# Performance work log

Hardware: AMD Instinct MI355X
Metric: run time of the kernel (lower is better)

The kernel has to match this reference:

```python
import jax, jax.numpy as jnp
import numpy as np

# Qwen3.5 GatedDeltaNet dims
B, T, HID = 2, 2048, 2048
HK, HV, DK, DV, KW = 16, 32, 128, 128, 4   # k-heads, v-heads, head dims, conv kernel
R = HV // HK                                # GQA repeat factor = 2
KEY_DIM = HK * DK                           # 2048
VAL_DIM = HV * DV                           # 4096
CONV_DIM = 2 * KEY_DIM + VAL_DIM            # 8192
EPS = 1e-6


def setup_inputs() -> dict:
    key = jax.random.key(0)
    ks = jax.random.split(key, 10)
    w = lambda k, shape, s=0.02: (jax.random.normal(k, shape) * s).astype(jnp.float32)
    A = jax.random.uniform(ks[8], (HV,), minval=1e-3, maxval=16.0)
    return {
        "hidden_states": jax.random.normal(ks[0], (B, T, HID), jnp.float32),
        "W_qkv": w(ks[1], (HID, CONV_DIM)),
        "W_z": w(ks[2], (HID, VAL_DIM)),
        "W_b": w(ks[3], (HID, HV)),
        "W_a": w(ks[4], (HID, HV)),
        "conv_w": w(ks[5], (CONV_DIM, KW), 0.5),   # depthwise causal conv taps
        "dt_bias": jnp.ones((HV,), jnp.float32),
        "A_log": jnp.log(A).astype(jnp.float32),
        "norm_weight": jnp.ones((DV,), jnp.float32),
        "W_out": w(ks[9], (VAL_DIM, HID)),
    }


def _forward(hidden_states, W_qkv, W_z, W_b, W_a, conv_w, dt_bias, A_log, norm_weight, W_out):
    x = hidden_states
    # --- projections ---
    qkv = x @ W_qkv                                    # [B,T,CONV_DIM]
    z = x @ W_z                                        # [B,T,VAL_DIM]
    beta = jax.nn.sigmoid(x @ W_b)                     # [B,T,HV]
    alpha = x @ W_a                                    # [B,T,HV]
    g = -jnp.exp(A_log) * jax.nn.softplus(alpha + dt_bias)  # [B,T,HV] (log-decay <= 0)

    # --- fix_query_key_value_ordering: per-k-head interleaved layout ---
    qkv = qkv.reshape(B, T, HK, 2 * DK + R * DV)
    q, k, v = jnp.split(qkv, [DK, 2 * DK], axis=3)
    mixed = jnp.concatenate([q.reshape(B, T, -1), k.reshape(B, T, -1), v.reshape(B, T, -1)], axis=-1)

    # --- causal depthwise short conv (kernel 4) + SiLU ---
    xp = jnp.pad(mixed, ((0, 0), (KW - 1, 0), (0, 0)))
    conv = sum(conv_w[:, i] * xp[:, i:i + T, :] for i in range(KW))
    conv = jax.nn.silu(conv)

    q, k, v = jnp.split(conv, [KEY_DIM, 2 * KEY_DIM], axis=-1)
    q = q.reshape(B, T, HK, DK)
    k = k.reshape(B, T, HK, DK)
    v = v.reshape(B, T, HV, DV)
    gate = z.reshape(B, T, HV, DV)

    # GQA: repeat q,k heads to match v heads
    q = jnp.repeat(q, R, axis=2)                       # [B,T,HV,DK]
    k = jnp.repeat(k, R, axis=2)

    # l2-norm q,k (use_qk_l2norm_in_kernel=True) and default scale 1/sqrt(DK)
    q = q / jnp.sqrt(jnp.sum(q * q, axis=-1, keepdims=True) + 1e-6)
    k = k / jnp.sqrt(jnp.sum(k * k, axis=-1, keepdims=True) + 1e-6)
    q = q * (DK ** -0.5)

    # --- gated delta rule recurrence (scan over time) ---
    # state S: [B,HV,DK,DV];  S_t = a_t*S_{t-1} + k_t (beta_t*(v_t - (a_t*S_{t-1})^T k_t))^T
    def step(S, inp):
        qt, kt, vt, gt, bt = inp                       # [B,HV,DK],[B,HV,DK],[B,HV,DV],[B,HV],[B,HV]
        S = S * jnp.exp(gt)[:, :, None, None]
        kv = jnp.einsum('bhk,bhkv->bhv', kt, S)
        delta = bt[..., None] * (vt - kv)              # [B,HV,DV]
        S = S + kt[..., None] * delta[:, :, None, :]
        o = jnp.einsum('bhk,bhkv->bhv', qt, S)
        return S, o

    tfirst = lambda a: jnp.moveaxis(a, 1, 0)           # [T,B,...]
    S0 = jnp.zeros((B, HV, DK, DV), q.dtype)
    _, o = jax.lax.scan(step, S0, (tfirst(q), tfirst(k), tfirst(v), tfirst(g), tfirst(beta)))
    o = jnp.moveaxis(o, 0, 1)                          # [B,T,HV,DV]

    # --- gated RMSNorm: rmsnorm(o) * silu(gate) * weight ---
    var = jnp.mean(o * o, axis=-1, keepdims=True)
    o = o * jax.lax.rsqrt(var + EPS)
    o = o * jax.nn.silu(gate)
    o = o * norm_weight

    return o.reshape(B, T, VAL_DIM) @ W_out            # [B,T,HID]


def reference(hidden_states, W_qkv, W_z, W_b, W_a, conv_w, dt_bias, A_log, norm_weight, W_out):
    return _forward(hidden_states, W_qkv, W_z, W_b, W_a, conv_w, dt_bias, A_log, norm_weight, W_out)
```

## Files before the change

### kernel.cpp

```cpp
#include <hip/hip_runtime.h>


#define T_LEN 2048
#define MROWS 4096

typedef __bf16 bf16x8 __attribute__((ext_vector_type(8)));
typedef float f32x4 __attribute__((ext_vector_type(4)));

#define MFMA(a, b, c) __builtin_amdgcn_mfma_f32_16x16x32_bf16((a), (b), (c), 0, 0, 0)

__device__ __forceinline__ unsigned short f2bf(float f) {
  unsigned int u = __float_as_uint(f);
  unsigned int r = (u + 0x7fffu + ((u >> 16) & 1u)) >> 16;
  return (unsigned short)r;
}
__device__ __forceinline__ float bf2f(unsigned short u) {
  return __uint_as_float(((unsigned int)u) << 16);
}
__device__ __forceinline__ void gload_lds16(const void* g, void* l) {
  __builtin_amdgcn_global_load_lds(
      (const __attribute__((address_space(1))) unsigned int*)g,
      (__attribute__((address_space(3))) unsigned int*)l, 16, 0, 0);
}

__global__ __launch_bounds__(256) void f32_to_bf16_vec(const float* __restrict__ src,
                                                       unsigned short* __restrict__ dst,
                                                       int n4) {
  int i = blockIdx.x * 256 + threadIdx.x;
  if (i >= n4) return;
  float4 v = ((const float4*)src)[i];
  ushort4 o;
  o.x = f2bf(v.x); o.y = f2bf(v.y); o.z = f2bf(v.z); o.w = f2bf(v.w);
  ((ushort4*)dst)[i] = o;
}

__global__ __launch_bounds__(256) void transpose_f2b(const float* __restrict__ src,
                                                     unsigned short* __restrict__ dst,
                                                     int R, int C) {
  __shared__ float tile[32][33];
  int tx = threadIdx.x & 31, ty = threadIdx.x >> 5;
  int c0 = blockIdx.x * 32, r0 = blockIdx.y * 32;
  #pragma unroll
  for (int i = ty; i < 32; i += 8)
    tile[i][tx] = src[(size_t)(r0 + i) * C + c0 + tx];
  __syncthreads();
  #pragma unroll
  for (int i = ty; i < 32; i += 8)
    dst[(size_t)(c0 + i) * R + r0 + tx] = f2bf(tile[tx][i]);
}

template <int OUTBF, int BN>
__global__ __launch_bounds__(512, 2) void gemm256(const unsigned short* __restrict__ A, int lda,
                                                  const unsigned short* __restrict__ Bt, int ldb,
                                                  void* __restrict__ Cv, int ldc,
                                                  int M, int N, int K) {
  constexpr int BUFSZ = 16384 + BN * 64;
  constexpr int BISS = BN / 64;
  constexpr int IS = 4 + BISS;
  constexpr int WMv = (BN == 256) ? 2 : 4;
  constexpr int MSUB = 256 / (WMv * 16);
  constexpr int MSPAN = 256 / WMv;

  __shared__ unsigned short lds[2 * BUFSZ];

  const int mtiles = M >> 8;
  const int nwg = gridDim.x;
  const int orig = blockIdx.x;
  const int q = nwg >> 3, r = nwg & 7;
  const int xcd = orig & 7, idx = orig >> 3;
  const int swz = (xcd < r ? xcd * (q + 1) : r * (q + 1) + (xcd - r) * q) + idx;
  const int m0 = (swz % mtiles) * 256;
  const int n0 = (swz / mtiles) * BN;

  const int tid = threadIdx.x, lane = tid & 63, wv = tid >> 6;
  const int wm = (BN == 256) ? (wv >> 2) : (wv >> 1);
  const int wn = (BN == 256) ? (wv & 3) : (wv & 1);
  const int l15 = lane & 15, l4 = lane >> 4;

  f32x4 acc[MSUB][4];
  #pragma unroll
  for (int i = 0; i < MSUB; i++)
    #pragma unroll
    for (int j = 0; j < 4; j++) acc[i][j] = f32x4{0.f, 0.f, 0.f, 0.f};

  const int NT = K >> 6;

  auto STAGE = [&](int kt) {
    unsigned short* base = lds + (kt & 1) * BUFSZ;
    const int k0 = kt << 6;
    #pragma unroll
    for (int is = 0; is < 4; is++) {
      int ow = is * 8192 + wv * 1024;
      int o = ow + lane * 16;
      int row = o >> 7, colB = o & 127;
      int scol = colB ^ ((row & 7) << 4);
      gload_lds16(A + (size_t)(m0 + row) * lda + k0 + (scol >> 1), base + (ow >> 1));
    }
    #pragma unroll
    for (int is = 0; is < BISS; is++) {
      int ow = is * 8192 + wv * 1024;
      int o = ow + lane * 16;
      int row = o >> 7, colB = o & 127;
      int scol = colB ^ ((row & 7) << 4);
      gload_lds16(Bt + (size_t)(n0 + row) * ldb + k0 + (scol >> 1), base + 16384 + (ow >> 1));
    }
  };

  STAGE(0);
  if (NT > 1) STAGE(1);
  if constexpr (IS == 8) asm volatile("s_waitcnt vmcnt(8)" ::: "memory");
  else                   asm volatile("s_waitcnt vmcnt(6)" ::: "memory");
  __builtin_amdgcn_sched_barrier(0);
  __builtin_amdgcn_s_barrier();
  __builtin_amdgcn_sched_barrier(0);

  for (int t = 0; t < NT; t++) {
    const unsigned short* Abuf = lds + (t & 1) * BUFSZ;
    const unsigned short* Bbuf = Abuf + 16384;
    bf16x8 bF[4][2];
    #pragma unroll
    for (int n = 0; n < 4; n++) {
      int rb = wn * 64 + n * 16 + l15;
      int sw = (rb & 7) << 4;
      #pragma unroll
      for (int ks = 0; ks < 2; ks++) {
        int colB = (ks * 32 + l4 * 8) * 2;
        bF[n][ks] = *(const bf16x8*)(Bbuf + rb * 64 + ((colB ^ sw) >> 1));
      }
    }
    __builtin_amdgcn_s_setprio(1);
    #pragma unroll
    for (int m = 0; m < MSUB; m++) {
      int ra = wm * MSPAN + m * 16 + l15;
      int sw = (ra & 7) << 4;
      int c0b = l4 * 16;
      bf16x8 a0 = *(const bf16x8*)(Abuf + ra * 64 + ((c0b ^ sw) >> 1));
      bf16x8 a1 = *(const bf16x8*)(Abuf + ra * 64 + (((64 + c0b) ^ sw) >> 1));
      #pragma unroll
      for (int n = 0; n < 4; n++) {
        acc[m][n] = MFMA(a0, bF[n][0], acc[m][n]);
        acc[m][n] = MFMA(a1, bF[n][1], acc[m][n]);
      }
    }
    __builtin_amdgcn_s_setprio(0);
    __builtin_amdgcn_sched_barrier(0);
    __builtin_amdgcn_s_barrier();
    __builtin_amdgcn_sched_barrier(0);
    if (t + 2 < NT) STAGE(t + 2);
    if (t + 1 < NT) {
      if (t + 2 < NT) {
        if constexpr (IS == 8) asm volatile("s_waitcnt vmcnt(8)" ::: "memory");
        else                   asm volatile("s_waitcnt vmcnt(6)" ::: "memory");
      } else {
        asm volatile("s_waitcnt vmcnt(0)" ::: "memory");
      }
      __builtin_amdgcn_sched_barrier(0);
      __builtin_amdgcn_s_barrier();
      __builtin_amdgcn_sched_barrier(0);
    }
  }

  #pragma unroll
  for (int m = 0; m < MSUB; m++) {
    int grow = m0 + wm * MSPAN + m * 16 + l4 * 4;
    #pragma unroll
    for (int n = 0; n < 4; n++) {
      int gcol = n0 + wn * 64 + n * 16 + l15;
      if (OUTBF) {
        unsigned short* cp = (unsigned short*)Cv + (size_t)grow * ldc + gcol;
        #pragma unroll
        for (int rr = 0; rr < 4; rr++) cp[(size_t)rr * ldc] = f2bf(acc[m][n][rr]);
      } else {
        float* cp = (float*)Cv + (size_t)grow * ldc + gcol;
        #pragma unroll
        for (int rr = 0; rr < 4; rr++) cp[(size_t)rr * ldc] = acc[m][n][rr];
      }
    }
  }
}

template <int OUTBF>
__global__ __launch_bounds__(256) void gemm_bf16(const unsigned short* __restrict__ A, int lda,
                                                 const unsigned short* __restrict__ Bt, int ldb,
                                                 void* __restrict__ Cv, int ldc,
                                                 int M, int N, int K) {
  __shared__ unsigned short As[128 * 64];
  __shared__ unsigned short Bs[128 * 64];
  const int tid = threadIdx.x, lane = tid & 63, wv = tid >> 6;
  const int wr = wv >> 1, wc = wv & 1;
  const int m0 = blockIdx.y * 128, n0 = blockIdx.x * 128;
  const int lrow8 = lane >> 3;
  const int lk8 = (lane & 7) * 8;

  f32x4 acc[4][4];
  #pragma unroll
  for (int i = 0; i < 4; i++)
    #pragma unroll
    for (int j = 0; j < 4; j++) acc[i][j] = f32x4{0.f, 0.f, 0.f, 0.f};

  for (int k0 = 0; k0 < K; k0 += 64) {
    #pragma unroll
    for (int j = 0; j < 4; ++j) {
      int chunk = j * 4 + wv;
      int r = chunk * 8 + lrow8;
      gload_lds16(A + (size_t)(m0 + r) * lda + k0 + lk8, (void*)(As + chunk * 512));
      gload_lds16(Bt + (size_t)(n0 + r) * ldb + k0 + lk8, (void*)(Bs + chunk * 512));
    }
    __syncthreads();
    #pragma unroll
    for (int half = 0; half < 2; ++half) {
      int ko = half * 32 + (lane >> 4) * 8;
      bf16x8 af[4], bfr[4];
      #pragma unroll
      for (int i = 0; i < 4; i++) {
        int ra = wr * 64 + i * 16 + (lane & 15);
        af[i] = *(const bf16x8*)(As + ra * 64 + ko);
        int rb = wc * 64 + i * 16 + (lane & 15);
        bfr[i] = *(const bf16x8*)(Bs + rb * 64 + ko);
      }
      #pragma unroll
      for (int i = 0; i < 4; i++)
        #pragma unroll
        for (int j = 0; j < 4; j++)
          acc[i][j] = MFMA(af[i], bfr[j], acc[i][j]);
    }
    __syncthreads();
  }
  int cr4 = (lane >> 4) * 4;
  int cc = lane & 15;
  #pragma unroll
  for (int i = 0; i < 4; i++) {
    int row = m0 + wr * 64 + i * 16 + cr4;
    #pragma unroll
    for (int j = 0; j < 4; j++) {
      int col = n0 + wc * 64 + j * 16 + cc;
      if (OUTBF) {
        unsigned short* cp = (unsigned short*)Cv + (size_t)row * ldc + col;
        #pragma unroll
        for (int r = 0; r < 4; r++) cp[(size_t)r * ldc] = f2bf(acc[i][j][r]);
      } else {
        float* cp = (float*)Cv + (size_t)row * ldc + col;
        #pragma unroll
        for (int r = 0; r < 4; r++) cp[(size_t)r * ldc] = acc[i][j][r];
      }
    }
  }
}

__global__ __launch_bounds__(256) void beta_g_kernel(const unsigned short* __restrict__ ba,
                                                     const float* __restrict__ A_log,
                                                     const float* __restrict__ dt_bias,
                                                     unsigned short* __restrict__ betab,
                                                     float* __restrict__ g) {
  int i = blockIdx.x * 256 + threadIdx.x;
  int row = i >> 5, hv = i & 31;
  float rb = bf2f(ba[(size_t)row * 128 + hv]);
  float ra = bf2f(ba[(size_t)row * 128 + 32 + hv]);
  betab[i] = f2bf(1.f / (1.f + expf(-rb)));
  float xg = ra + dt_bias[hv];
  float sp = (xg > 20.f) ? xg : log1pf(expf(xg));
  g[i] = -expf(A_log[hv]) * sp;
}

__global__ __launch_bounds__(256) void conv_kernel(const unsigned short* __restrict__ qkv,
                                                   const float* __restrict__ conv_w,
                                                   unsigned short* __restrict__ out) {
  const int seg = blockIdx.x, tt = blockIdx.y, b = blockIdx.z;
  const int tid = threadIdx.x;
  const int c0 = seg * 128;
  const bool isq = seg < 16;
  int scb;
  if (isq) scb = seg * 512;
  else if (seg < 32) scb = (seg - 16) * 512 + 128;
  else scb = ((seg - 32) >> 1) * 512 + 256 + ((seg - 32) & 1) * 128;

  __shared__ unsigned short raw[35][136];
  __shared__ float cw[4][132];

  for (int i = tid; i < 512; i += 256) {
    int cl = i >> 2, tap = i & 3;
    cw[tap][cl] = conv_w[(size_t)(c0 + cl) * 4 + tap];
  }
  const int t0 = tt * 32;
  for (int i = tid; i < 560; i += 256) {
    int row = i >> 4, col = (i & 15) * 8;
    int gt = t0 - 3 + row;
    uint4 v = make_uint4(0u, 0u, 0u, 0u);
    if (gt >= 0) v = *(const uint4*)(qkv + (size_t)(b * T_LEN + gt) * 8192 + scb + col);
    *(uint4*)(&raw[row][col]) = v;
  }
  __syncthreads();
  const int s = tid >> 3, dg = tid & 7;
  union RawU { uint4 v[2]; unsigned short h[16]; };
  RawU u[4];
  #pragma unroll
  for (int i = 0; i < 4; i++) {
    const uint4* p = (const uint4*)&raw[s + i][dg * 16];
    u[i].v[0] = p[0]; u[i].v[1] = p[1];
  }
  float vals[16]; float ss = 0.f;
  #pragma unroll
  for (int j = 0; j < 16; j++) {
    float a = 0.f;
    #pragma unroll
    for (int i = 0; i < 4; i++) a = fmaf(cw[i][dg * 16 + j], bf2f(u[i].h[j]), a);
    a = a / (1.f + expf(-a));
    vals[j] = a; ss += a * a;
  }
  if (seg < 32) {
    ss += __shfl_xor(ss, 1); ss += __shfl_xor(ss, 2); ss += __shfl_xor(ss, 4);
    float sc = rsqrtf(ss + 1e-6f);
    if (isq) sc *= 0.08838834764831845f;
    #pragma unroll
    for (int j = 0; j < 16; j++) vals[j] *= sc;
  }
  union { uint4 v[2]; unsigned short h[16]; } ov;
  #pragma unroll
  for (int j = 0; j < 16; j++) ov.h[j] = f2bf(vals[j]);
  unsigned short* op = out + (size_t)(b * T_LEN + t0 + s) * 8192 + c0 + dg * 16;
  *(uint4*)(op) = ov.v[0];
  *(uint4*)(op + 8) = ov.v[1];
}

__global__ __launch_bounds__(256) void prep_kernel(const unsigned short* __restrict__ conv,
                                                   const float* __restrict__ g,
                                                   const unsigned short* __restrict__ betab,
                                                   unsigned short* __restrict__ M1g,
                                                   unsigned short* __restrict__ M2g,
                                                   unsigned char* __restrict__ vecs) {
  const int c = blockIdx.x, bh = blockIdx.y;
  const int b = bh >> 5, hv = bh & 31, hk = hv >> 1;
  const int bhc = bh * 32 + c;
  const int tid = threadIdx.x, lane = tid & 63, wv = tid >> 6;
  const int r0 = b * T_LEN + c * 64;
  const int l15 = lane & 15, l4 = lane >> 4;

  __shared__ unsigned short Kb[128 * 72];
  __shared__ unsigned short QbX[64 * 136];
  __shared__ unsigned short Lbf[64 * 72];
  __shared__ unsigned short Pb[64 * 72];
  __shared__ unsigned short WT[3 * 16 * 40];
  __shared__ float Gs[64], SCs[64], BLs[64];

  unsigned short* Qb = QbX;
  unsigned short* XTb = QbX;
  unsigned short* Xdrow = QbX + 4608;

  if (wv == 0) {
    float gt = g[(size_t)(r0 + lane) * 32 + hv];
    #pragma unroll
    for (int d = 1; d < 64; d <<= 1) {
      float o = __shfl_up(gt, (unsigned)d, 64);
      if (lane >= d) gt += o;
    }
    float GC = __shfl(gt, 63, 64);
    float lam = expf(gt);
    float beta = bf2f(betab[(size_t)(r0 + lane) * 32 + hv]);
    Gs[lane] = gt;
    SCs[lane] = expf(GC - gt);
    BLs[lane] = beta;
    unsigned short* vb16 = (unsigned short*)(vecs + (size_t)bhc * 272);
    vb16[lane] = f2bf(beta * lam);
    vb16[64 + lane] = f2bf(lam);
    if (lane == 0) *(float*)(vecs + (size_t)bhc * 272 + 256) = expf(GC);
  }
  const unsigned short* Kg = conv + (size_t)r0 * 8192 + 2048 + hk * 128;
  const unsigned short* Qg = conv + (size_t)r0 * 8192 + hk * 128;
  for (int u = tid; u < 1024; u += 256) {
    int row = u >> 4, col = (u & 15) * 8;
    *(uint4*)(&Kb[row * 136 + col]) = *(const uint4*)(Kg + (size_t)row * 8192 + col);
    *(uint4*)(&Qb[row * 136 + col]) = *(const uint4*)(Qg + (size_t)row * 8192 + col);
  }
  __syncthreads();

  {
    f32x4 akk[4], aqk[4];
    #pragma unroll
    for (int st = 0; st < 4; st++) { akk[st] = f32x4{0,0,0,0}; aqk[st] = f32x4{0,0,0,0}; }
    int trow = wv * 16 + l15;
    int klo = l4 * 8;
    #pragma unroll
    for (int ks = 0; ks < 4; ks++) {
      int ko = ks * 32 + klo;
      bf16x8 ak = *(const bf16x8*)(&Kb[trow * 136 + ko]);
      bf16x8 aq = *(const bf16x8*)(&Qb[trow * 136 + ko]);
      #pragma unroll
      for (int st = 0; st < 4; st++) {
        bf16x8 bk = *(const bf16x8*)(&Kb[(st * 16 + l15) * 136 + ko]);
        akk[st] = MFMA(ak, bk, akk[st]);
        aqk[st] = MFMA(aq, bk, aqk[st]);
      }
    }
    int orow = wv * 16 + l4 * 4;
    int oc = l15;
    #pragma unroll
    for (int st = 0; st < 4; st++)
      #pragma unroll
      for (int r = 0; r < 4; r++) {
        int t = orow + r, ssv = st * 16 + oc;
        float e = expf(fminf(Gs[t] - Gs[ssv], 0.f));
        Lbf[t * 72 + ssv] = f2bf((ssv < t) ? BLs[t] * e * akk[st][r] : 0.f);
        Pb[t * 72 + ssv] = f2bf((ssv <= t) ? e * aqk[st][r] : 0.f);
      }
  }
  __syncthreads();

  unsigned short ktv[32];
  {
    int dk = tid >> 1, tb = (tid & 1) * 32;
    #pragma unroll
    for (int i = 0; i < 32; i++)
      ktv[i] = f2bf(bf2f(Kb[(tb + i) * 136 + dk]) * SCs[tb + i]);
    for (int u = tid; u < 896; u += 256) {
      *(uint4*)(&QbX[u * 8]) = make_uint4(0u, 0u, 0u, 0u);
    }
    for (int u = tid; u < 240; u += 256) {
      *(uint4*)(&WT[u * 8]) = make_uint4(0u, 0u, 0u, 0u);
    }
  }
  __syncthreads();

  {
    int dk = tid >> 1, tb = (tid & 1) * 32;
    #pragma unroll
    for (int i = 0; i < 32; i++) Kb[dk * 72 + tb + i] = ktv[i];
  }
  {
    const int w16 = wv * 16;
    const int cc = l15;
    float xr[16];
    #pragma unroll
    for (int t = 0; t < 16; t++) {
      float acc = (cc == t) ? 1.f : 0.f;
      union { uint4 v[2]; unsigned short h[16]; } rw;
      const uint4* p = (const uint4*)(&Lbf[(w16 + t) * 72 + w16]);
      rw.v[0] = p[0]; rw.v[1] = p[1];
      #pragma unroll
      for (int s = 0; s < 16; s++) {
        if (s < t) acc = fmaf(-bf2f(rw.h[s]), xr[s], acc);
      }
      xr[t] = acc;
    }
    if (lane < 16) {
      #pragma unroll
      for (int t = 0; t < 16; t++) {
        unsigned short v = f2bf(xr[t]);
        XTb[(w16 + cc) * 72 + w16 + t] = v;
        Xdrow[wv * 640 + t * 40 + cc] = v;
      }
    }
  }
  __syncthreads();

  if (wv < 3) {
    const int j = wv;
    for (int i = j + 1; i < 4; i++) {
      f32x4 w_ = f32x4{0.f, 0.f, 0.f, 0.f};
      #pragma unroll
      for (int ks = 0; ks < 2; ks++) {
        int so = ks * 32 + l4 * 8;
        bf16x8 af = *(const bf16x8*)(&Lbf[(i * 16 + l15) * 72 + so]);
        bf16x8 bfv = *(const bf16x8*)(&XTb[(j * 16 + l15) * 72 + so]);
        w_ = MFMA(af, bfv, w_);
      }
      #pragma unroll
      for (int r = 0; r < 4; r++)
        WT[j * 640 + l15 * 40 + l4 * 4 + r] = f2bf(-w_[r]);
      f32x4 xij = f32x4{0.f, 0.f, 0.f, 0.f};
      {
        bf16x8 af = *(const bf16x8*)(&Xdrow[i * 640 + l15 * 40 + l4 * 8]);
        bf16x8 bfv = *(const bf16x8*)(&WT[j * 640 + l15 * 40 + l4 * 8]);
        xij = MFMA(af, bfv, xij);
      }
      #pragma unroll
      for (int r = 0; r < 4; r++)
        XTb[(j * 16 + l15) * 72 + i * 16 + l4 * 4 + r] = f2bf(xij[r]);
    }
  }
  __syncthreads();

  for (int tt = wv * 12; tt < wv * 12 + 12; tt++) {
    f32x4 acc = f32x4{0, 0, 0, 0};
    const unsigned short* Abase;
    int mrow, jc;
    if (tt < 16) { mrow = (tt >> 2) * 16; jc = (tt & 3) * 16; Abase = Pb + mrow * 72; }
    else { int i2 = tt - 16; mrow = (i2 >> 2) * 16; jc = (i2 & 3) * 16; Abase = Kb + mrow * 72; }
    #pragma unroll
    for (int ks = 0; ks < 2; ks++) {
      int so = ks * 32 + l4 * 8;
      bf16x8 af = *(const bf16x8*)(Abase + l15 * 72 + so);
      bf16x8 bfv = *(const bf16x8*)(&XTb[(jc + l15) * 72 + so]);
      acc = MFMA(af, bfv, acc);
    }
    int ro = mrow + l4 * 4, co = jc + l15;
    if (tt < 16) {
      #pragma unroll
      for (int r = 0; r < 4; r++)
        M1g[(size_t)bhc * 4096 + (ro + r) * 64 + co] = f2bf(acc[r]);
    } else {
      #pragma unroll
      for (int r = 0; r < 4; r++)
        M2g[(size_t)bhc * 8192 + (ro + r) * 64 + co] = f2bf(acc[r]);
    }
  }
}

__global__ __launch_bounds__(512) void seq_kernel(unsigned short* __restrict__ conv,
                                                  const unsigned short* __restrict__ M1g,
                                                  const unsigned short* __restrict__ M2g,
                                                  const unsigned char* __restrict__ vecs,
                                                  const unsigned short* __restrict__ betab) {
  const int dvs = blockIdx.x, bh = blockIdx.y;
  const int b = bh >> 5, hv = bh & 31, hk = hv >> 1;
  const int dv0 = dvs * 32;
  const int tid = threadIdx.x, lane = tid & 63, wv = tid >> 6;

  __shared__ unsigned short Kb[64 * 136], Qb[64 * 136];
  __shared__ float Sf[128 * 36];
  __shared__ unsigned short S0T[32 * 136];
  __shared__ unsigned short rhsT[32 * 72];

  for (int i = tid; i < 128 * 36; i += 512) Sf[i] = 0.f;
  for (int i = tid; i < 32 * 136; i += 512) S0T[i] = 0;
  __syncthreads();

  const int l15 = lane & 15, l4 = lane >> 4;
  const int trt = (wv >> 1) * 16;
  const int tct = (wv & 1) * 16;

  for (int c = 0; c < 32; c++) {
    const int r0 = b * T_LEN + c * 64;
    const int bhc = bh * 32 + c;
    const unsigned char* vb = vecs + (size_t)bhc * 272;
    const unsigned short* vb16 = (const unsigned short*)vb;
    #pragma unroll
    for (int j = 0; j < 2; j++) {
      int u = tid * 2 + j;
      int row = u >> 4, col = (u & 15) * 8;
      uint4 kv = *(const uint4*)(conv + (size_t)(r0 + row) * 8192 + 2048 + hk * 128 + col);
      uint4 qv = *(const uint4*)(conv + (size_t)(r0 + row) * 8192 + hk * 128 + col);
      *(uint4*)(&Kb[row * 136 + col]) = kv;
      float lam = bf2f(vb16[64 + row]);
      union { uint4 u4; unsigned short h[8]; } qq; qq.u4 = qv;
      #pragma unroll
      for (int e = 0; e < 8; e++) qq.h[e] = f2bf(bf2f(qq.h[e]) * lam);
      *(uint4*)(&Qb[row * 136 + col]) = qq.u4;
    }
    __syncthreads();
    {
      f32x4 acc = f32x4{0, 0, 0, 0};
      #pragma unroll
      for (int ks = 0; ks < 4; ks++) {
        int ko = ks * 32 + l4 * 8;
        bf16x8 af = *(const bf16x8*)(&Kb[(trt + l15) * 136 + ko]);
        bf16x8 bfv = *(const bf16x8*)(&S0T[(tct + l15) * 136 + ko]);
        acc = MFMA(af, bfv, acc);
      }
      #pragma unroll
      for (int r = 0; r < 4; r++) {
        int tl = trt + l4 * 4 + r;
        int t = r0 + tl;
        float beta = bf2f(betab[(size_t)t * 32 + hv]);
        float bl = bf2f(vb16[tl]);
        float vv = bf2f(conv[(size_t)t * 8192 + 4096 + hv * 128 + dv0 + tct + l15]);
        rhsT[(tct + l15) * 72 + tl] = f2bf(beta * vv - bl * acc[r]);
      }
    }
    __syncthreads();
    {
      f32x4 acc = f32x4{0, 0, 0, 0};
      const unsigned short* m1b = M1g + (size_t)bhc * 4096;
      #pragma unroll
      for (int ks = 0; ks < 2; ks++) {
        int so = ks * 32 + l4 * 8;
        union { uint4 u4; bf16x8 h; } af;
        af.u4 = *(const uint4*)(m1b + (trt + l15) * 64 + so);
        bf16x8 bfv = *(const bf16x8*)(&rhsT[(tct + l15) * 72 + so]);
        acc = MFMA(af.h, bfv, acc);
      }
      #pragma unroll
      for (int ks = 0; ks < 4; ks++) {
        int ko = ks * 32 + l4 * 8;
        bf16x8 af = *(const bf16x8*)(&Qb[(trt + l15) * 136 + ko]);
        bf16x8 bfv = *(const bf16x8*)(&S0T[(tct + l15) * 136 + ko]);
        acc = MFMA(af, bfv, acc);
      }
      #pragma unroll
      for (int r = 0; r < 4; r++) {
        int t = r0 + trt + l4 * 4 + r;
        conv[(size_t)t * 8192 + 4096 + hv * 128 + dv0 + tct + l15] = f2bf(acc[r]);
      }
    }
    {
      float lamC = *(const float*)(vb + 256);
      f32x4 sacc[2];
      const unsigned short* m2b = M2g + (size_t)bhc * 8192;
      const int dkb = wv * 16;
      #pragma unroll
      for (int dt = 0; dt < 2; dt++) {
        int dvb = dt * 16;
        f32x4 a;
        #pragma unroll
        for (int r = 0; r < 4; r++) a[r] = lamC * Sf[(dkb + l4 * 4 + r) * 36 + dvb + l15];
        #pragma unroll
        for (int ks = 0; ks < 2; ks++) {
          int so = ks * 32 + l4 * 8;
          union { uint4 u4; bf16x8 h; } af;
          af.u4 = *(const uint4*)(m2b + (dkb + l15) * 64 + so);
          bf16x8 bfv = *(const bf16x8*)(&rhsT[(dvb + l15) * 72 + so]);
          a = MFMA(af.h, bfv, a);
        }
        sacc[dt] = a;
      }
      __syncthreads();
      #pragma unroll
      for (int dt = 0; dt < 2; dt++) {
        int dvb = dt * 16;
        #pragma unroll
        for (int r = 0; r < 4; r++) {
          int dk = dkb + l4 * 4 + r, dvl = dvb + l15;
          Sf[dk * 36 + dvl] = sacc[dt][r];
          S0T[dvl * 136 + dk] = f2bf(sacc[dt][r]);
        }
      }
    }
    __syncthreads();
  }
}

__global__ __launch_bounds__(256) void rmsgate_kernel(unsigned short* __restrict__ conv,
                                                      const unsigned short* __restrict__ zg,
                                                      const float* __restrict__ nw) {
  int wid = blockIdx.x * 4 + (threadIdx.x >> 6);
  int lane = threadIdx.x & 63;
  int row = wid >> 5, hv = wid & 31;
  unsigned short* op = conv + (size_t)row * 8192 + 4096 + hv * 128;
  float o0 = bf2f(op[lane]), o1 = bf2f(op[64 + lane]);
  float ss = o0 * o0 + o1 * o1;
  #pragma unroll
  for (int m = 1; m < 64; m <<= 1) ss += __shfl_xor(ss, m);
  float r = rsqrtf(ss * (1.f / 128.f) + 1e-6f);
  const unsigned short* zp = zg + (size_t)row * 4096 + hv * 128;
  float g0 = bf2f(zp[lane]), g1 = bf2f(zp[64 + lane]);
  g0 = g0 / (1.f + expf(-g0));
  g1 = g1 / (1.f + expf(-g1));
  op[lane] = f2bf(o0 * r * g0 * nw[lane]);
  op[64 + lane] = f2bf(o1 * r * g1 * nw[64 + lane]);
}

extern "C" void kernel_launch(void* const* d_in, const int* in_sizes, int n_in,
                              void* d_out, int out_size, void* d_ws, size_t ws_size,
                              hipStream_t stream) {
  (void)in_sizes; (void)n_in; (void)out_size;
  const float* x       = (const float*)d_in[0];
  const float* W_qkv   = (const float*)d_in[1];
  const float* W_z     = (const float*)d_in[2];
  const float* W_b     = (const float*)d_in[3];
  const float* W_a     = (const float*)d_in[4];
  const float* conv_w  = (const float*)d_in[5];
  const float* dt_bias = (const float*)d_in[6];
  const float* A_log   = (const float*)d_in[7];
  const float* nw      = (const float*)d_in[8];
  const float* W_out   = (const float*)d_in[9];
  float* out = (float*)d_out;

  const size_t NEED = 169115648ULL;
  if (ws_size < NEED) return;

  char* ws = (char*)d_ws;
  unsigned short* qkv_bf = (unsigned short*)(ws + 0);
  unsigned short* M1g    = (unsigned short*)(ws + 0);
  unsigned short* M2g    = (unsigned short*)(ws + 16777216);
  unsigned short* WoutT  = (unsigned short*)(ws + 0);
  unsigned short* zg     = (unsigned short*)(ws + 67108864);
  unsigned short* WzT    = (unsigned short*)(ws + 100663296);
  unsigned short* x_bf   = (unsigned short*)(ws + 100663296 + 16777216);
  unsigned short* WqkvT  = (unsigned short*)(ws + 100663296 + 33554432);
  unsigned short* WbaT   = (unsigned short*)(ws + 100663296 + 33554432);
  unsigned short* ba     = (unsigned short*)(ws + 100663296 + 34078720);
  unsigned short* convb  = (unsigned short*)(ws + 100663296);
  unsigned short* betab  = (unsigned short*)(ws + 167772160);
  float* gbuf            = (float*)(ws + 168034304);
  unsigned char* vecs    = (unsigned char*)(ws + 168558592);

  const int M = MROWS;

  f32_to_bf16_vec<<<(M * 2048 / 4) / 256, 256, 0, stream>>>(x, x_bf, M * 2048 / 4);
  transpose_f2b<<<dim3(8192 / 32, 2048 / 32), 256, 0, stream>>>(W_qkv, WqkvT, 2048, 8192);
  transpose_f2b<<<dim3(4096 / 32, 2048 / 32), 256, 0, stream>>>(W_z, WzT, 2048, 4096);

  gemm256<1, 256><<<512, 512, 0, stream>>>(x_bf, 2048, WqkvT, 2048, qkv_bf, 8192, M, 8192, 2048);

  transpose_f2b<<<dim3(1, 64), 256, 0, stream>>>(W_b, WbaT, 2048, 32);
  transpose_f2b<<<dim3(1, 64), 256, 0, stream>>>(W_a, WbaT + (size_t)32 * 2048, 2048, 32);

  gemm256<1, 256><<<256, 512, 0, stream>>>(x_bf, 2048, WzT, 2048, zg, 4096, M, 4096, 2048);
  gemm_bf16<1><<<dim3(1, M / 128), 256, 0, stream>>>(x_bf, 2048, WbaT, 2048, ba, 128, M, 128, 2048);

  beta_g_kernel<<<(M * 32) / 256, 256, 0, stream>>>(ba, A_log, dt_bias, betab, gbuf);

  conv_kernel<<<dim3(64, 64, 2), 256, 0, stream>>>(qkv_bf, conv_w, convb);

  prep_kernel<<<dim3(32, 64), 256, 0, stream>>>(convb, gbuf, betab, M1g, M2g, vecs);

  seq_kernel<<<dim3(4, 64), 512, 0, stream>>>(convb, M1g, M2g, vecs, betab);

  rmsgate_kernel<<<32768, 256, 0, stream>>>(convb, zg, nw);

  transpose_f2b<<<dim3(2048 / 32, 4096 / 32), 256, 0, stream>>>(W_out, WoutT, 4096, 2048);
  gemm256<0, 128><<<256, 512, 0, stream>>>(convb + 4096, 8192, WoutT, 4096, out, 2048, M, 2048, 4096);
}
```

Baseline: 621.7 us.

## Split sequential delta-rule kernel into 16-wide DV slices across more blocks

```diff
diff --git a/kernel.cpp b/kernel.cpp
--- a/kernel.cpp
+++ b/kernel.cpp
@@ -505,28 +505,27 @@
   }
 }
 
-__global__ __launch_bounds__(512) void seq_kernel(unsigned short* __restrict__ conv,
+__global__ __launch_bounds__(256) void seq_kernel(unsigned short* __restrict__ conv,
                                                   const unsigned short* __restrict__ M1g,
                                                   const unsigned short* __restrict__ M2g,
                                                   const unsigned char* __restrict__ vecs,
                                                   const unsigned short* __restrict__ betab) {
   const int dvs = blockIdx.x, bh = blockIdx.y;
   const int b = bh >> 5, hv = bh & 31, hk = hv >> 1;
-  const int dv0 = dvs * 32;
+  const int dv0 = dvs * 16;
   const int tid = threadIdx.x, lane = tid & 63, wv = tid >> 6;
 
   __shared__ unsigned short Kb[64 * 136], Qb[64 * 136];
-  __shared__ float Sf[128 * 36];
-  __shared__ unsigned short S0T[32 * 136];
-  __shared__ unsigned short rhsT[32 * 72];
-
-  for (int i = tid; i < 128 * 36; i += 512) Sf[i] = 0.f;
-  for (int i = tid; i < 32 * 136; i += 512) S0T[i] = 0;
+  __shared__ float Sf[128 * 20];
+  __shared__ unsigned short S0T[16 * 136];
+  __shared__ unsigned short rhsT[16 * 72];
+
+  for (int i = tid; i < 128 * 20; i += 256) Sf[i] = 0.f;
+  for (int i = tid; i < 16 * 136; i += 256) S0T[i] = 0;
   __syncthreads();
 
   const int l15 = lane & 15, l4 = lane >> 4;
-  const int trt = (wv >> 1) * 16;
-  const int tct = (wv & 1) * 16;
+  const int trt = wv * 16;
 
   for (int c = 0; c < 32; c++) {
     const int r0 = b * T_LEN + c * 64;
@@ -534,8 +533,8 @@
     const unsigned char* vb = vecs + (size_t)bhc * 272;
     const unsigned short* vb16 = (const unsigned short*)vb;
     #pragma unroll
-    for (int j = 0; j < 2; j++) {
-      int u = tid * 2 + j;
+    for (int j = 0; j < 4; j++) {
+      int u = j * 256 + tid;
       int row = u >> 4, col = (u & 15) * 8;
       uint4 kv = *(const uint4*)(conv + (size_t)(r0 + row) * 8192 + 2048 + hk * 128 + col);
       uint4 qv = *(const uint4*)(conv + (size_t)(r0 + row) * 8192 + hk * 128 + col);
@@ -553,7 +552,7 @@
       for (int ks = 0; ks < 4; ks++) {
         int ko = ks * 32 + l4 * 8;
         bf16x8 af = *(const bf16x8*)(&Kb[(trt + l15) * 136 + ko]);
-        bf16x8 bfv = *(const bf16x8*)(&S0T[(tct + l15) * 136 + ko]);
+        bf16x8 bfv = *(const bf16x8*)(&S0T[l15 * 136 + ko]);
         acc = MFMA(af, bfv, acc);
       }
       #pragma unroll
@@ -562,8 +561,8 @@
         int t = r0 + tl;
         float beta = bf2f(betab[(size_t)t * 32 + hv]);
         float bl = bf2f(vb16[tl]);
-        float vv = bf2f(conv[(size_t)t * 8192 + 4096 + hv * 128 + dv0 + tct + l15]);
-        rhsT[(tct + l15) * 72 + tl] = f2bf(beta * vv - bl * acc[r]);
+        float vv = bf2f(conv[(size_t)t * 8192 + 4096 + hv * 128 + dv0 + l15]);
+        rhsT[l15 * 72 + tl] = f2bf(beta * vv - bl * acc[r]);
       }
     }
     __syncthreads();
@@ -575,52 +574,51 @@
         int so = ks * 32 + l4 * 8;
         union { uint4 u4; bf16x8 h; } af;
         af.u4 = *(const uint4*)(m1b + (trt + l15) * 64 + so);
-        bf16x8 bfv = *(const bf16x8*)(&rhsT[(tct + l15) * 72 + so]);
+        bf16x8 bfv = *(const bf16x8*)(&rhsT[l15 * 72 + so]);
         acc = MFMA(af.h, bfv, acc);
       }
       #pragma unroll
       for (int ks = 0; ks < 4; ks++) {
         int ko = ks * 32 + l4 * 8;
         bf16x8 af = *(const bf16x8*)(&Qb[(trt + l15) * 136 + ko]);
-        bf16x8 bfv = *(const bf16x8*)(&S0T[(tct + l15) * 136 + ko]);
+        bf16x8 bfv = *(const bf16x8*)(&S0T[l15 * 136 + ko]);
         acc = MFMA(af, bfv, acc);
       }
       #pragma unroll
       for (int r = 0; r < 4; r++) {
         int t = r0 + trt + l4 * 4 + r;
-        conv[(size_t)t * 8192 + 4096 + hv * 128 + dv0 + tct + l15] = f2bf(acc[r]);
+        conv[(size_t)t * 8192 + 4096 + hv * 128 + dv0 + l15] = f2bf(acc[r]);
       }
     }
     {
       float lamC = *(const float*)(vb + 256);
       f32x4 sacc[2];
       const unsigned short* m2b = M2g + (size_t)bhc * 8192;
-      const int dkb = wv * 16;
-      #pragma unroll
-      for (int dt = 0; dt < 2; dt++) {
-        int dvb = dt * 16;
+      #pragma unroll
+      for (int dkt = 0; dkt < 2; dkt++) {
+        int dkb = (wv * 2 + dkt) * 16;
         f32x4 a;
         #pragma unroll
-        for (int r = 0; r < 4; r++) a[r] = lamC * Sf[(dkb + l4 * 4 + r) * 36 + dvb + l15];
+        for (int r = 0; r < 4; r++) a[r] = lamC * Sf[(dkb + l4 * 4 + r) * 20 + l15];
         #pragma unroll
         for (int ks = 0; ks < 2; ks++) {
           int so = ks * 32 + l4 * 8;
           union { uint4 u4; bf16x8 h; } af;
           af.u4 = *(const uint4*)(m2b + (dkb + l15) * 64 + so);
-          bf16x8 bfv = *(const bf16x8*)(&rhsT[(dvb + l15) * 72 + so]);
+          bf16x8 bfv = *(const bf16x8*)(&rhsT[l15 * 72 + so]);
           a = MFMA(af.h, bfv, a);
         }
-        sacc[dt] = a;
+        sacc[dkt] = a;
       }
       __syncthreads();
       #pragma unroll
-      for (int dt = 0; dt < 2; dt++) {
-        int dvb = dt * 16;
+      for (int dkt = 0; dkt < 2; dkt++) {
+        int dkb = (wv * 2 + dkt) * 16;
         #pragma unroll
         for (int r = 0; r < 4; r++) {
-          int dk = dkb + l4 * 4 + r, dvl = dvb + l15;
-          Sf[dk * 36 + dvl] = sacc[dt][r];
-          S0T[dvl * 136 + dk] = f2bf(sacc[dt][r]);
+          int dk = dkb + l4 * 4 + r;
+          Sf[dk * 20 + l15] = sacc[dkt][r];
+          S0T[l15 * 136 + dk] = f2bf(sacc[dkt][r]);
         }
       }
     }
@@ -703,7 +701,7 @@
 
   prep_kernel<<<dim3(32, 64), 256, 0, stream>>>(convb, gbuf, betab, M1g, M2g, vecs);
 
-  seq_kernel<<<dim3(4, 64), 512, 0, stream>>>(convb, M1g, M2g, vecs, betab);
+  seq_kernel<<<dim3(8, 64), 256, 0, stream>>>(convb, M1g, M2g, vecs, betab);
 
   rmsgate_kernel<<<32768, 256, 0, stream>>>(convb, zg, nw);
 
```

After: 627.0 us. No clear change (+0.8%).
